# Kernel tuning notes

Measured on AMD Instinct MI355X. Metric: run time of the kernel, lower is better.

Reference implementation:

```python
import jax, jax.numpy as jnp
import numpy as np

N, C, T, H, W = 8, 3, 32, 256, 256
K = 5  # kernel size, pad = K // 2 ('same' output size)


def _dw_conv_last(x2, w):
    """Depthwise 1D cross-correlation along last axis.
    x2: [B, C, L], w: [C, K] -> [B, C, L] (zero 'same' padding).
    Matches torch.nn.Conv1d(groups=C, bias=False, padding=K//2)."""
    pad = w.shape[1] // 2
    return jax.lax.conv_general_dilated(
        x2, w[:, None, :],  # kernel [O=C, I=1, K]
        window_strides=(1,), padding=[(pad, pad)],
        dimension_numbers=('NCH', 'OIH', 'NCH'),
        feature_group_count=w.shape[0])


def _conv_along(x, w, axis):
    """Depthwise conv of [N,C,T,H,W] along `axis` (2, 3 or 4)."""
    y = jnp.moveaxis(x, axis, -1)   # [N, C, a, b, L]
    y = jnp.moveaxis(y, 1, -2)      # [N, a, b, C, L]
    sh = y.shape
    y = _dw_conv_last(y.reshape(-1, sh[3], sh[4]), w).reshape(sh)
    y = jnp.moveaxis(y, -2, 1)      # [N, C, a, b, L]
    return jnp.moveaxis(y, -1, axis)


def setup_inputs() -> dict:
    key = jax.random.key(0)
    kx, k1, k2, k3 = jax.random.split(key, 4)
    return {
        'x': jax.random.normal(kx, (N, C, T, H, W), dtype=jnp.float32),
        'w1': jax.random.normal(k1, (C, K), dtype=jnp.float32),  # along W
        'w2': jax.random.normal(k2, (C, K), dtype=jnp.float32),  # along H
        'w3': jax.random.normal(k3, (C, K), dtype=jnp.float32),  # along T
    }


def reference(x, w1, w2, w3):
    # Axis-separable depthwise 3D conv: W, then H, then T (as in SeparableConv3D).
    x = _conv_along(x, w1, 4)
    x = _conv_along(x, w2, 3)
    x = _conv_along(x, w3, 2)
    return x  # [N, C, T, H, W]
```

## Files before the change

### kernel.cpp

```cpp
#include <hip/hip_runtime.h>


#define N_  8
#define C_  3
#define T_  32
#define H_  256
#define W_  256
#define K_  5
#define HW_ (H_ * W_)

#define TH 16
#define TW 64
#define XSTR 68
#define XF2  272
#define XPADF 640

typedef float nfloat4 __attribute__((ext_vector_type(4)));

__global__ __launch_bounds__(256)
void sep3d_wave(const float* __restrict__ x,
                const float* __restrict__ w1,
                const float* __restrict__ w2,
                const float* __restrict__ w3,
                float* __restrict__ out)
{
    __shared__ float sxAll[4][2][XPADF];

    const int tid = threadIdx.x;
    const int wv  = tid >> 6;
    const int ln  = tid & 63;
    const int nc  = blockIdx.z;
    const int c   = nc % C_;
    const int h0  = blockIdx.y * TH + wv * 4;
    const int w0  = blockIdx.x * TW;

    const float* xnc = x   + (size_t)nc * (T_ * HW_);
    float*       onc = out + (size_t)nc * (T_ * HW_);

    float k1[K_], k2[K_], k3[K_];
#pragma unroll
    for (int k = 0; k < K_; ++k) {
        k1[k] = w1[c * K_ + k];
        k2[k] = w2[c * K_ + k];
        k3[k] = w3[c * K_ + k];
    }

    int  goff[5];
    bool gok[5];
    int  loff[5];
#pragma unroll
    for (int j = 0; j < 5; ++j) {
        int i   = ln + 64 * j;
        int row = i / 34;
        int c2  = i - row * 34;
        int gh  = h0 - 2 + row;
        int gw  = w0 - 2 + 2 * c2;
        gok[j]  = (i < XF2) && ((unsigned)gh < H_) && (gw >= 0) && (gw + 1 < W_);
        goff[j] = gok[j] ? (gh * W_ + gw) : 0;
        loff[j] = 2 * i;
    }

    const int r0 = ln >> 4;
    const int s3 = ln & 15;
    float* gst = onc + (size_t)(h0 + r0) * W_ + (w0 + 4 * s3);

    nfloat4 a0 = {0,0,0,0}, a1 = a0, a2 = a0, a3 = a0;

    float2 pA[5], pB[5];

#define LOADP(P, tt) do {                                                   \
    const int tc_ = ((tt) < T_) ? (tt) : 0;                                 \
    const bool tok_ = (tt) < T_;                                            \
    const float* xt_ = xnc + (size_t)tc_ * HW_;                             \
    _Pragma("unroll") for (int j = 0; j < 5; ++j) {                         \
        float2 v_ = *(const float2*)(xt_ + goff[j]);                        \
        bool ok_ = tok_ && gok[j];                                          \
        (P)[j].x = ok_ ? v_.x : 0.0f;                                       \
        (P)[j].y = ok_ ? v_.y : 0.0f;                                       \
    } } while (0)

#define WRITEP(P, B) do {                                                   \
    float* sw_ = &sxAll[wv][(B)][0];                                        \
    _Pragma("unroll") for (int j = 0; j < 5; ++j)                           \
        *(float2*)(sw_ + loff[j]) = (P)[j];                                 \
    } while (0)

#define COMPUTE(B, tt) do {                                                 \
    const float* sr_ = &sxAll[wv][(B)][0];                                  \
    nfloat4 z = {0,0,0,0};                                                  \
    _Pragma("unroll") for (int k = 0; k < K_; ++k) {                        \
        const float4* pp = (const float4*)(sr_ + (r0 + k) * XSTR + 4 * s3); \
        float4 aa = pp[0], bb = pp[1];                                      \
        float y0 = aa.x*k1[0]+aa.y*k1[1]+aa.z*k1[2]+aa.w*k1[3]+bb.x*k1[4];  \
        float y1 = aa.y*k1[0]+aa.z*k1[1]+aa.w*k1[2]+bb.x*k1[3]+bb.y*k1[4];  \
        float y2 = aa.z*k1[0]+aa.w*k1[1]+bb.x*k1[2]+bb.y*k1[3]+bb.z*k1[4];  \
        float y3 = aa.w*k1[0]+bb.x*k1[1]+bb.y*k1[2]+bb.z*k1[3]+bb.w*k1[4];  \
        z.x += y0 * k2[k]; z.y += y1 * k2[k];                               \
        z.z += y2 * k2[k]; z.w += y3 * k2[k];                               \
    }                                                                       \
    nfloat4 dn;                                                             \
    dn.x = a0.x + z.x * k3[4]; dn.y = a0.y + z.y * k3[4];                   \
    dn.z = a0.z + z.z * k3[4]; dn.w = a0.w + z.w * k3[4];                   \
    if ((tt) >= 2)                                                          \
        __builtin_nontemporal_store(dn,                                     \
            (nfloat4*)(gst + (size_t)((tt) - 2) * HW_));                    \
    a0.x = a1.x + z.x * k3[3]; a0.y = a1.y + z.y * k3[3];                   \
    a0.z = a1.z + z.z * k3[3]; a0.w = a1.w + z.w * k3[3];                   \
    a1.x = a2.x + z.x * k3[2]; a1.y = a2.y + z.y * k3[2];                   \
    a1.z = a2.z + z.z * k3[2]; a1.w = a2.w + z.w * k3[2];                   \
    a2.x = a3.x + z.x * k3[1]; a2.y = a3.y + z.y * k3[1];                   \
    a2.z = a3.z + z.z * k3[1]; a2.w = a3.w + z.w * k3[1];                   \
    a3.x = z.x * k3[0]; a3.y = z.y * k3[0];                                 \
    a3.z = z.z * k3[0]; a3.w = z.w * k3[0];                                 \
    } while (0)

    LOADP(pA, 0);
    WRITEP(pA, 0);
    LOADP(pA, 1);
    LOADP(pB, 2);

    for (int t = 0; t < T_; t += 2) {
        COMPUTE(0, t);
        WRITEP(pA, 1);
        LOADP(pA, t + 3);
        COMPUTE(1, t + 1);
        WRITEP(pB, 0);
        LOADP(pB, t + 4);
    }

    __builtin_nontemporal_store(a0, (nfloat4*)(gst + (size_t)30 * HW_));
    __builtin_nontemporal_store(a1, (nfloat4*)(gst + (size_t)31 * HW_));

#undef LOADP
#undef WRITEP
#undef COMPUTE
}

extern "C" void kernel_launch(void* const* d_in, const int* in_sizes, int n_in,
                              void* d_out, int out_size, void* d_ws, size_t ws_size,
                              hipStream_t stream)
{
    const float* x  = (const float*)d_in[0];
    const float* w1 = (const float*)d_in[1];
    const float* w2 = (const float*)d_in[2];
    const float* w3 = (const float*)d_in[3];
    float* out = (float*)d_out;

    dim3 grid(W_ / TW, H_ / TH, N_ * C_);
    sep3d_wave<<<grid, 256, 0, stream>>>(x, w1, w2, w3, out);
}
```

Before: 375.9 us.

## Replace double-buffered LDS tile with split A/B halo layout for conflict-free float4 reads

Reorganizes each wave's LDS staging from two padded 68-stride buffers into a single buffer with two 64-stride copies (A covering columns 0..63 and B shifted by 4), so each lane's window reads become two aligned float4 loads at unit lane stride. Every loaded float2 is written twice, with out-of-range entries routed to a dump region, which removes the double buffer at the cost of more LDS writes. Launch bounds now request 6 blocks per SM. With a single buffer per wave, correctness relies on the wave's lanes executing in lockstep between reads and the following writes, since there is no barrier.

```diff
diff --git a/kernel.cpp b/kernel.cpp
--- a/kernel.cpp
+++ b/kernel.cpp
@@ -11,20 +11,22 @@
 
 #define TH 16
 #define TW 64
-#define XSTR 68
-#define XF2  272
-#define XPADF 640
+
+#define ABASE 0
+#define BBASE 512
+#define DBASE 1024
+#define REG_F 1152
 
 typedef float nfloat4 __attribute__((ext_vector_type(4)));
 
-__global__ __launch_bounds__(256)
-void sep3d_wave(const float* __restrict__ x,
-                const float* __restrict__ w1,
-                const float* __restrict__ w2,
-                const float* __restrict__ w3,
-                float* __restrict__ out)
+__global__ __launch_bounds__(256, 6)
+void sep3d_wave5(const float* __restrict__ x,
+                 const float* __restrict__ w1,
+                 const float* __restrict__ w2,
+                 const float* __restrict__ w3,
+                 float* __restrict__ out)
 {
-    __shared__ float sxAll[4][2][XPADF];
+    __shared__ __align__(16) float sxAll[4][REG_F];
 
     const int tid = threadIdx.x;
     const int wv  = tid >> 6;
@@ -45,24 +47,32 @@
         k3[k] = w3[c * K_ + k];
     }
 
+    float* base = &sxAll[wv][0];
+
     int  goff[5];
     bool gok[5];
-    int  loff[5];
+    int  loffA[5], loffB[5];
 #pragma unroll
     for (int j = 0; j < 5; ++j) {
-        int i   = ln + 64 * j;
-        int row = i / 34;
-        int c2  = i - row * 34;
-        int gh  = h0 - 2 + row;
-        int gw  = w0 - 2 + 2 * c2;
-        gok[j]  = (i < XF2) && ((unsigned)gh < H_) && (gw >= 0) && (gw + 1 < W_);
-        goff[j] = gok[j] ? (gh * W_ + gw) : 0;
-        loff[j] = 2 * i;
+        int i    = ln + 64 * j;
+        int row  = i / 34;
+        int c2   = i - row * 34;
+        int e    = 2 * c2;
+        int gh   = h0 - 2 + row;
+        int gw   = w0 - 2 + e;
+        bool valid = (i < 272);
+        gok[j]   = valid && ((unsigned)gh < H_) && (gw >= 0) && (gw + 1 < W_);
+        goff[j]  = gok[j] ? (gh * W_ + gw) : 0;
+        int lr   = row * 64 + e;
+        int dmp  = DBASE + 2 * ln;
+        loffA[j] = (valid && e <= 62) ? (ABASE + lr)     : dmp;
+        loffB[j] = (valid && e >= 4)  ? (BBASE + lr - 4) : dmp;
     }
 
     const int r0 = ln >> 4;
     const int s3 = ln & 15;
     float* gst = onc + (size_t)(h0 + r0) * W_ + (w0 + 4 * s3);
+    const float* rd = base + 4 * ln;
 
     nfloat4 a0 = {0,0,0,0}, a1 = a0, a2 = a0, a3 = a0;
 
@@ -79,18 +89,17 @@
         (P)[j].y = ok_ ? v_.y : 0.0f;                                       \
     } } while (0)
 
-#define WRITEP(P, B) do {                                                   \
-    float* sw_ = &sxAll[wv][(B)][0];                                        \
-    _Pragma("unroll") for (int j = 0; j < 5; ++j)                           \
-        *(float2*)(sw_ + loff[j]) = (P)[j];                                 \
-    } while (0)
+#define WRITEP(P) do {                                                      \
+    _Pragma("unroll") for (int j = 0; j < 5; ++j) {                         \
+        *(float2*)(base + loffA[j]) = (P)[j];                               \
+        *(float2*)(base + loffB[j]) = (P)[j];                               \
+    } } while (0)
 
-#define COMPUTE(B, tt) do {                                                 \
-    const float* sr_ = &sxAll[wv][(B)][0];                                  \
+#define COMPUTE(tt) do {                                                    \
     nfloat4 z = {0,0,0,0};                                                  \
     _Pragma("unroll") for (int k = 0; k < K_; ++k) {                        \
-        const float4* pp = (const float4*)(sr_ + (r0 + k) * XSTR + 4 * s3); \
-        float4 aa = pp[0], bb = pp[1];                                      \
+        float4 aa = *(const float4*)(rd + 64 * k);                          \
+        float4 bb = *(const float4*)(rd + BBASE + 64 * k);                  \
         float y0 = aa.x*k1[0]+aa.y*k1[1]+aa.z*k1[2]+aa.w*k1[3]+bb.x*k1[4];  \
         float y1 = aa.y*k1[0]+aa.z*k1[1]+aa.w*k1[2]+bb.x*k1[3]+bb.y*k1[4];  \
         float y2 = aa.z*k1[0]+aa.w*k1[1]+bb.x*k1[2]+bb.y*k1[3]+bb.z*k1[4];  \
@@ -115,16 +124,16 @@
     } while (0)
 
     LOADP(pA, 0);
-    WRITEP(pA, 0);
+    WRITEP(pA);
     LOADP(pA, 1);
     LOADP(pB, 2);
 
     for (int t = 0; t < T_; t += 2) {
-        COMPUTE(0, t);
-        WRITEP(pA, 1);
+        COMPUTE(t);
+        WRITEP(pA);
         LOADP(pA, t + 3);
-        COMPUTE(1, t + 1);
-        WRITEP(pB, 0);
+        COMPUTE(t + 1);
+        WRITEP(pB);
         LOADP(pB, t + 4);
     }
 
@@ -147,5 +156,5 @@
     float* out = (float*)d_out;
 
     dim3 grid(W_ / TW, H_ / TH, N_ * C_);
-    sep3d_wave<<<grid, 256, 0, stream>>>(x, w1, w2, w3, out);
+    sep3d_wave5<<<grid, 256, 0, stream>>>(x, w1, w2, w3, out);
 }
```

New measurement: 933.4 us. +148.3%, slower.
